# Performance work log

Measured on AMD Instinct MI355X. Metric: run time of the kernel, lower is better.

Reference implementation:

```python
import jax, jax.numpy as jnp
import numpy as np

N_NODES = 100000
N_EDGES = 1600000
NUM_FEATURES = 128


def setup_inputs() -> dict:
    key = jax.random.key(0)
    ks = jax.random.split(key, 10)
    x = jax.random.normal(ks[0], (N_NODES, NUM_FEATURES), dtype=jnp.float32)
    edge_index = jax.random.randint(ks[1], (2, N_EDGES), 0, N_NODES, dtype=jnp.int64)
    # conv1 MLP: Linear(num_features,128) -> ReLU -> Linear(128,128)
    s1 = 1.0 / np.sqrt(NUM_FEATURES)
    W1 = jax.random.uniform(ks[2], (NUM_FEATURES, 128), jnp.float32, -s1, s1)
    b1 = jax.random.uniform(ks[3], (128,), jnp.float32, -s1, s1)
    s2 = 1.0 / np.sqrt(128)
    W2 = jax.random.uniform(ks[4], (128, 128), jnp.float32, -s2, s2)
    b2 = jax.random.uniform(ks[5], (128,), jnp.float32, -s2, s2)
    # conv2 MLP: Linear(128,64) -> ReLU -> Linear(64,64)
    W3 = jax.random.uniform(ks[6], (128, 64), jnp.float32, -s2, s2)
    b3 = jax.random.uniform(ks[7], (64,), jnp.float32, -s2, s2)
    s3 = 1.0 / np.sqrt(64)
    W4 = jax.random.uniform(ks[8], (64, 64), jnp.float32, -s3, s3)
    b4 = jax.random.uniform(ks[9], (64,), jnp.float32, -s3, s3)
    return {"x": x, "edge_index": edge_index, "W1": W1, "b1": b1,
            "W2": W2, "b2": b2, "W3": W3, "b3": b3, "W4": W4, "b4": b4}


def _gin_conv(x, src, dst, Wa, ba, Wb, bb):
    # GINConv with eps=0: out = MLP(x + sum_{j->i} x_j)
    agg = jax.ops.segment_sum(x[src], dst, num_segments=N_NODES)
    h = x + agg
    h = jax.nn.relu(h @ Wa + ba)
    return h @ Wb + bb


def reference(x, edge_index, W1, b1, W2, b2, W3, b3, W4, b4):
    src, dst = edge_index[0], edge_index[1]
    h = jax.nn.relu(_gin_conv(x, src, dst, W1, b1, W2, b2))
    h = jax.nn.relu(_gin_conv(h, src, dst, W3, b3, W4, b4))
    return h
```

## Files before the change

### kernel.cpp

```cpp
#include <hip/hip_runtime.h>
#include <hip/hip_bf16.h>

#define NODES 100000
#define EDGES 1600000
#define NBINS ((NODES + 127) >> 7)
#define BINCAP 4096
#define PB_BLOCKS 256
#define PB_CHUNK ((EDGES + PB_BLOCKS - 1) / PB_BLOCKS)
#define CAST_BLOCKS 12500
#define WPREP_BLOCKS 176

typedef __bf16 bf16x8 __attribute__((ext_vector_type(8)));
typedef float f32x4 __attribute__((ext_vector_type(4)));

__device__ __forceinline__ unsigned short f2b(float f) {
  __hip_bfloat16 h = __float2bfloat16(f);
  return __builtin_bit_cast(unsigned short, h);
}
__device__ __forceinline__ float b_lo(unsigned u) { return __uint_as_float(u << 16); }
__device__ __forceinline__ float b_hi(unsigned u) { return __uint_as_float(u & 0xffff0000u); }

__global__ __launch_bounds__(256) void prep_count(
    const float4* __restrict__ x4, ushort4* __restrict__ xh4,
    const float* __restrict__ W1, const float* __restrict__ W2,
    const float* __restrict__ W3, const float* __restrict__ W4,
    unsigned short* __restrict__ Wt1, unsigned short* __restrict__ Wt2,
    unsigned short* __restrict__ Wt3, unsigned short* __restrict__ Wt4,
    const int* __restrict__ dst, int* __restrict__ partialT) {
  __shared__ int h[NBINS];
  const int b = blockIdx.x;
  if (b < CAST_BLOCKS) {
    int i = b * 256 + threadIdx.x;
    float4 v = x4[i];
    ushort4 o;
    o.x = f2b(v.x); o.y = f2b(v.y); o.z = f2b(v.z); o.w = f2b(v.w);
    xh4[i] = o;
    return;
  }
  if (b < CAST_BLOCKS + WPREP_BLOCKS) {
    int i = (b - CAST_BLOCKS) * 256 + threadIdx.x;
    if (i < 16384) {
      int n = i >> 7, k = i & 127;
      Wt1[i] = f2b(W1[k * 128 + n]);
    } else if (i < 32768) {
      int j = i - 16384; int n = j >> 7, k = j & 127;
      Wt2[j] = f2b(W2[k * 128 + n]);
    } else if (i < 40960) {
      int j = i - 32768; int n = j >> 7, k = j & 127;
      Wt3[j] = f2b(W3[k * 64 + n]);
    } else if (i < 45056) {
      int j = i - 40960; int n = j >> 6, k = j & 63;
      Wt4[j] = f2b(W4[k * 64 + n]);
    }
    return;
  }
  const int cb = b - CAST_BLOCKS - WPREP_BLOCKS;
  for (int i = threadIdx.x; i < NBINS; i += 256) h[i] = 0;
  __syncthreads();
  const int beg = cb * PB_CHUNK;
  const int end = min(beg + PB_CHUNK, EDGES);
  for (int e = beg + threadIdx.x; e < end; e += 256)
    atomicAdd(&h[dst[e] >> 7], 1);
  __syncthreads();
  for (int i = threadIdx.x; i < NBINS; i += 256)
    partialT[i * PB_BLOCKS + cb] = h[i];
}

__global__ __launch_bounds__(256) void scan_blockoff(const int* __restrict__ partialT,
                                                     int* __restrict__ blockoffT,
                                                     int* __restrict__ binTotal) {
  __shared__ int s[256];
  const int bin = blockIdx.x;
  const int t = threadIdx.x;
  int v = partialT[bin * PB_BLOCKS + t];
  s[t] = v;
  __syncthreads();
  for (int off = 1; off < 256; off <<= 1) {
    int u = (t >= off) ? s[t - off] : 0;
    __syncthreads();
    s[t] += u;
    __syncthreads();
  }
  blockoffT[bin * PB_BLOCKS + t] = s[t] - v;
  if (t == 255) binTotal[bin] = s[255];
}

__global__ __launch_bounds__(1024) void scan_totals(const int* __restrict__ binTotal,
                                                    int* __restrict__ binStart,
                                                    int* __restrict__ rowstart) {
  __shared__ int s[1024];
  const int t = threadIdx.x;
  int v = (t < NBINS) ? binTotal[t] : 0;
  s[t] = v;
  __syncthreads();
  for (int off = 1; off < 1024; off <<= 1) {
    int u = (t >= off) ? s[t - off] : 0;
    __syncthreads();
    s[t] += u;
    __syncthreads();
  }
  if (t < NBINS) binStart[t] = s[t] - v;
  if (t == 0) {
    binStart[NBINS] = EDGES;
    rowstart[NODES] = EDGES;
  }
}

__global__ __launch_bounds__(256) void bin_scatter(const int* __restrict__ src,
                                                   const int* __restrict__ dst,
                                                   const int* __restrict__ binStart,
                                                   const int* __restrict__ blockoffT,
                                                   unsigned* __restrict__ coarse) {
  __shared__ int base[NBINS];
  __shared__ int h[NBINS];
  const int beg = blockIdx.x * PB_CHUNK;
  const int end = min(beg + PB_CHUNK, EDGES);
  for (int i = threadIdx.x; i < NBINS; i += 256) {
    base[i] = binStart[i] + blockoffT[i * PB_BLOCKS + blockIdx.x];
    h[i] = 0;
  }
  __syncthreads();
  for (int e = beg + threadIdx.x; e < end; e += 256) {
    int d = dst[e];
    int b = d >> 7;
    int pos = base[b] + atomicAdd(&h[b], 1);
    coarse[pos] = (unsigned)src[e] | ((unsigned)(d & 127) << 17);
  }
}

__global__ __launch_bounds__(256) void bin_fine(const unsigned* __restrict__ coarse,
                                                const int* __restrict__ binStart,
                                                int* __restrict__ rowstart,
                                                int* __restrict__ bucket) {
  __shared__ unsigned ent[BINCAP];
  __shared__ unsigned obuf[BINCAP];
  __shared__ int deg[128];
  __shared__ int pre[128];
  const int b = blockIdx.x;
  const int t = threadIdx.x;
  const int s0 = binStart[b];
  const int nE = binStart[b + 1] - s0;
  const int binBase = b << 7;

  if (t < 128) deg[t] = 0;
  __syncthreads();
  for (int i = t; i < nE; i += 256) {
    unsigned e = coarse[s0 + i];
    ent[i] = e;
    atomicAdd(&deg[e >> 17], 1);
  }
  __syncthreads();
  int v = 0;
  if (t < 128) {
    v = deg[t];
    pre[t] = v;
  }
  __syncthreads();
  for (int off = 1; off < 128; off <<= 1) {
    int u = (t >= off && t < 128) ? pre[t - off] : 0;
    __syncthreads();
    if (t < 128) pre[t] += u;
    __syncthreads();
  }
  if (t < 128) {
    int ex = pre[t] - v;
    if (binBase + t < NODES) rowstart[binBase + t] = s0 + ex;
    deg[t] = ex;
  }
  __syncthreads();
  for (int i = t; i < nE; i += 256) {
    unsigned e = ent[i];
    int pos = atomicAdd(&deg[e >> 17], 1);
    obuf[pos] = e & 0x1FFFFu;
  }
  __syncthreads();
  for (int i = t; i < nE; i += 256) bucket[s0 + i] = (int)obuf[i];
}

__global__ __launch_bounds__(256) void gather_sum_bf16(
    const uint4* __restrict__ xq, const int* __restrict__ rowstart,
    const int* __restrict__ bucket, uint4* __restrict__ outq) {
  const int n = blockIdx.x * 4 + (threadIdx.x >> 6);
  if (n >= NODES) return;
  const int lane = threadIdx.x & 63;
  const int g = lane >> 4;
  const int fl = lane & 15;

  float a[8] = {0.f, 0.f, 0.f, 0.f, 0.f, 0.f, 0.f, 0.f};
  if (g == 0) {
    uint4 v = xq[(size_t)n * 16 + fl];
    a[0] = b_lo(v.x); a[1] = b_hi(v.x);
    a[2] = b_lo(v.y); a[3] = b_hi(v.y);
    a[4] = b_lo(v.z); a[5] = b_hi(v.z);
    a[6] = b_lo(v.w); a[7] = b_hi(v.w);
  }

  const int beg = rowstart[n];
  const int end = rowstart[n + 1];
  for (int j = beg; j < end; j += 16) {
    int e0 = j + g, e1 = j + 4 + g, e2 = j + 8 + g, e3 = j + 12 + g;
    int i0 = (e0 < end) ? e0 : (end - 1);
    int i1 = (e1 < end) ? e1 : (end - 1);
    int i2 = (e2 < end) ? e2 : (end - 1);
    int i3 = (e3 < end) ? e3 : (end - 1);
    int s0 = bucket[i0], s1 = bucket[i1], s2 = bucket[i2], s3 = bucket[i3];
    uint4 v0 = xq[(size_t)s0 * 16 + fl];
    uint4 v1 = xq[(size_t)s1 * 16 + fl];
    uint4 v2 = xq[(size_t)s2 * 16 + fl];
    uint4 v3 = xq[(size_t)s3 * 16 + fl];
    float m0 = (e0 < end) ? 1.f : 0.f;
    float m1 = (e1 < end) ? 1.f : 0.f;
    float m2 = (e2 < end) ? 1.f : 0.f;
    float m3 = (e3 < end) ? 1.f : 0.f;
    a[0] = fmaf(b_lo(v0.x), m0, a[0]); a[1] = fmaf(b_hi(v0.x), m0, a[1]);
    a[2] = fmaf(b_lo(v0.y), m0, a[2]); a[3] = fmaf(b_hi(v0.y), m0, a[3]);
    a[4] = fmaf(b_lo(v0.z), m0, a[4]); a[5] = fmaf(b_hi(v0.z), m0, a[5]);
    a[6] = fmaf(b_lo(v0.w), m0, a[6]); a[7] = fmaf(b_hi(v0.w), m0, a[7]);
    a[0] = fmaf(b_lo(v1.x), m1, a[0]); a[1] = fmaf(b_hi(v1.x), m1, a[1]);
    a[2] = fmaf(b_lo(v1.y), m1, a[2]); a[3] = fmaf(b_hi(v1.y), m1, a[3]);
    a[4] = fmaf(b_lo(v1.z), m1, a[4]); a[5] = fmaf(b_hi(v1.z), m1, a[5]);
    a[6] = fmaf(b_lo(v1.w), m1, a[6]); a[7] = fmaf(b_hi(v1.w), m1, a[7]);
    a[0] = fmaf(b_lo(v2.x), m2, a[0]); a[1] = fmaf(b_hi(v2.x), m2, a[1]);
    a[2] = fmaf(b_lo(v2.y), m2, a[2]); a[3] = fmaf(b_hi(v2.y), m2, a[3]);
    a[4] = fmaf(b_lo(v2.z), m2, a[4]); a[5] = fmaf(b_hi(v2.z), m2, a[5]);
    a[6] = fmaf(b_lo(v2.w), m2, a[6]); a[7] = fmaf(b_hi(v2.w), m2, a[7]);
    a[0] = fmaf(b_lo(v3.x), m3, a[0]); a[1] = fmaf(b_hi(v3.x), m3, a[1]);
    a[2] = fmaf(b_lo(v3.y), m3, a[2]); a[3] = fmaf(b_hi(v3.y), m3, a[3]);
    a[4] = fmaf(b_lo(v3.z), m3, a[4]); a[5] = fmaf(b_hi(v3.z), m3, a[5]);
    a[6] = fmaf(b_lo(v3.w), m3, a[6]); a[7] = fmaf(b_hi(v3.w), m3, a[7]);
  }

#pragma unroll
  for (int k = 0; k < 8; k++) {
    a[k] += __shfl_xor(a[k], 16, 64);
    a[k] += __shfl_xor(a[k], 32, 64);
  }

  if (lane < 16) {
    uint4 o;
    o.x = ((unsigned)f2b(a[1]) << 16) | f2b(a[0]);
    o.y = ((unsigned)f2b(a[3]) << 16) | f2b(a[2]);
    o.z = ((unsigned)f2b(a[5]) << 16) | f2b(a[4]);
    o.w = ((unsigned)f2b(a[7]) << 16) | f2b(a[6]);
    outq[(size_t)n * 16 + fl] = o;
  }
}

template <int K, int N1, int N2, bool OUT_F32>
__global__ __launch_bounds__(256, 3) void mlp_fused(
    const unsigned short* __restrict__ A,
    const unsigned short* __restrict__ Wa, const float* __restrict__ ba,
    const unsigned short* __restrict__ Wb, const float* __restrict__ bb,
    void* __restrict__ Cout, int M) {
  constexpr int LDA = K + 8;
  constexpr int LWA = K + 8;
  constexpr int LWB = N1 + 8;
  constexpr int NT1 = N1 / 16, KB1 = K / 32;
  constexpr int NT2 = N2 / 16, KB2 = N1 / 32;
  constexpr int WSH = (N1 * LWA > N2 * LWB) ? N1 * LWA : N2 * LWB;
  __shared__ unsigned short S[64 * LDA];
  __shared__ unsigned short Wl[WSH];

  const int tid = threadIdx.x;
  const int wave = tid >> 6;
  const int lane = tid & 63;
  const int g = lane >> 4;
  const int fl = lane & 15;
  const int rowBase = blockIdx.x * 64;

  for (int i = tid; i < 64 * (K / 8); i += 256) {
    int r = i / (K / 8), c = i % (K / 8);
    uint4 v = make_uint4(0, 0, 0, 0);
    if (rowBase + r < M)
      v = ((const uint4*)A)[(size_t)(rowBase + r) * (K / 8) + c];
    *(uint4*)&S[r * LDA + c * 8] = v;
  }
  for (int i = tid; i < N1 * (K / 8); i += 256) {
    int n = i / (K / 8), c = i % (K / 8);
    *(uint4*)&Wl[n * LWA + c * 8] = *(const uint4*)&Wa[(size_t)n * K + c * 8];
  }
  __syncthreads();

  const int arow = wave * 16 + fl;

  f32x4 acc[NT1];
#pragma unroll
  for (int c = 0; c < NT1; c++) acc[c] = (f32x4){0.f, 0.f, 0.f, 0.f};
#pragma unroll
  for (int kb = 0; kb < KB1; kb++) {
    bf16x8 av = *(const bf16x8*)&S[arow * LDA + kb * 32 + g * 8];
#pragma unroll
    for (int c = 0; c < NT1; c++) {
      bf16x8 bv = *(const bf16x8*)&Wl[(c * 16 + fl) * LWA + kb * 32 + g * 8];
      acc[c] = __builtin_amdgcn_mfma_f32_16x16x32_bf16(av, bv, acc[c], 0, 0, 0);
    }
  }

#pragma unroll
  for (int c = 0; c < NT1; c++) {
    int col = c * 16 + fl;
    float bv = ba[col];
#pragma unroll
    for (int reg = 0; reg < 4; reg++) {
      int rloc = wave * 16 + g * 4 + reg;
      S[rloc * LDA + col] = f2b(fmaxf(acc[c][reg] + bv, 0.f));
    }
  }
  __syncthreads();

  for (int i = tid; i < N2 * (N1 / 8); i += 256) {
    int n = i / (N1 / 8), c = i % (N1 / 8);
    *(uint4*)&Wl[n * LWB + c * 8] = *(const uint4*)&Wb[(size_t)n * N1 + c * 8];
  }
  __syncthreads();

  f32x4 acc2[NT2];
#pragma unroll
  for (int c = 0; c < NT2; c++) acc2[c] = (f32x4){0.f, 0.f, 0.f, 0.f};
#pragma unroll
  for (int kb = 0; kb < KB2; kb++) {
    bf16x8 av = *(const bf16x8*)&S[arow * LDA + kb * 32 + g * 8];
#pragma unroll
    for (int c = 0; c < NT2; c++) {
      bf16x8 bv = *(const bf16x8*)&Wl[(c * 16 + fl) * LWB + kb * 32 + g * 8];
      acc2[c] = __builtin_amdgcn_mfma_f32_16x16x32_bf16(av, bv, acc2[c], 0, 0, 0);
    }
  }

#pragma unroll
  for (int c = 0; c < NT2; c++) {
    int col = c * 16 + fl;
    float bv = bb[col];
#pragma unroll
    for (int reg = 0; reg < 4; reg++) {
      int row = rowBase + wave * 16 + g * 4 + reg;
      if (row < M) {
        float v = fmaxf(acc2[c][reg] + bv, 0.f);
        if (OUT_F32)
          ((float*)Cout)[(size_t)row * N2 + col] = v;
        else
          ((unsigned short*)Cout)[(size_t)row * N2 + col] = f2b(v);
      }
    }
  }
}

extern "C" void kernel_launch(void* const* d_in, const int* in_sizes, int n_in,
                              void* d_out, int out_size, void* d_ws, size_t ws_size,
                              hipStream_t stream) {
  const float* x = (const float*)d_in[0];
  const int* ei = (const int*)d_in[1];
  const int* src = ei;
  const int* dst = ei + EDGES;
  const float* W1 = (const float*)d_in[2];
  const float* b1 = (const float*)d_in[3];
  const float* W2 = (const float*)d_in[4];
  const float* b2 = (const float*)d_in[5];
  const float* W3 = (const float*)d_in[6];
  const float* b3 = (const float*)d_in[7];
  const float* W4 = (const float*)d_in[8];
  const float* b4 = (const float*)d_in[9];
  float* out = (float*)d_out;

  char* ws = (char*)d_ws;
  unsigned short* xh = (unsigned short*)ws;
  unsigned short* hA = xh + (size_t)NODES * 128;
  unsigned short* hB = hA + (size_t)NODES * 128;
  unsigned short* Wt1 = hB + (size_t)NODES * 128;
  unsigned short* Wt2 = Wt1 + 128 * 128;
  unsigned short* Wt3 = Wt2 + 128 * 128;
  unsigned short* Wt4 = Wt3 + 64 * 128;
  int* rowstart = (int*)(Wt4 + 64 * 64);
  int* binStart = rowstart + NODES + 1;
  int* binTotal = binStart + NBINS + 1;
  int* partialT = binTotal + NBINS;
  int* blockoffT = partialT + NBINS * PB_BLOCKS;
  unsigned* coarse = (unsigned*)(blockoffT + NBINS * PB_BLOCKS);
  int* bucket = (int*)(coarse + EDGES);

  const int nblocks4 = (NODES + 3) / 4;
  const int gblocks = (NODES + 63) / 64;

  prep_count<<<CAST_BLOCKS + WPREP_BLOCKS + PB_BLOCKS, 256, 0, stream>>>(
      (const float4*)x, (ushort4*)xh, W1, W2, W3, W4, Wt1, Wt2, Wt3, Wt4,
      dst, partialT);
  scan_blockoff<<<NBINS, 256, 0, stream>>>(partialT, blockoffT, binTotal);
  scan_totals<<<1, 1024, 0, stream>>>(binTotal, binStart, rowstart);
  bin_scatter<<<PB_BLOCKS, 256, 0, stream>>>(src, dst, binStart, blockoffT, coarse);
  bin_fine<<<NBINS, 256, 0, stream>>>(coarse, binStart, rowstart, bucket);

  gather_sum_bf16<<<nblocks4, 256, 0, stream>>>((const uint4*)xh, rowstart, bucket,
                                                (uint4*)hA);
  mlp_fused<128, 128, 128, false><<<gblocks, 256, 0, stream>>>(
      hA, Wt1, b1, Wt2, b2, hB, NODES);

  gather_sum_bf16<<<nblocks4, 256, 0, stream>>>((const uint4*)hB, rowstart, bucket,
                                                (uint4*)hA);
  mlp_fused<128, 64, 64, true><<<gblocks, 256, 0, stream>>>(
      hA, Wt3, b3, Wt4, b4, out, NODES);
}
```

Baseline: 341.0 us.

## Gather features in column-chunked bf16 layout so each slice fits in cache

Node features are now stored in a chunk-major layout: 8 slices of 16 bf16 columns, each slice 3.2 MB. The gather kernel processes one slice per block group (blockIdx & 7), so the random source-row reads hit a working set small enough for L2/LLC. The cast, the MLP input load and the hidden-layer store are rewritten to use this layout. The cost is re-reading the CSR indices eight times, with more blocks and shorter per-lane 32-byte loads. It also uses nontemporal loads for the index streams.

```diff
diff --git a/kernel.cpp b/kernel.cpp
--- a/kernel.cpp
+++ b/kernel.cpp
@@ -10,8 +10,13 @@
 #define CAST_BLOCKS 12500
 #define WPREP_BLOCKS 176
 
+#define NCHUNK 8
+#define CHUNK_U4 (NODES * 2)
+#define GS_BLOCKS (NCHUNK * (NODES / 16))
+
 typedef __bf16 bf16x8 __attribute__((ext_vector_type(8)));
 typedef float f32x4 __attribute__((ext_vector_type(4)));
+typedef unsigned u32x4 __attribute__((ext_vector_type(4)));
 
 __device__ __forceinline__ unsigned short f2b(float f) {
   __hip_bfloat16 h = __float2bfloat16(f);
@@ -30,11 +35,15 @@
   __shared__ int h[NBINS];
   const int b = blockIdx.x;
   if (b < CAST_BLOCKS) {
-    int i = b * 256 + threadIdx.x;
-    float4 v = x4[i];
-    ushort4 o;
-    o.x = f2b(v.x); o.y = f2b(v.y); o.z = f2b(v.z); o.w = f2b(v.w);
-    xh4[i] = o;
+    int o = b * 256 + threadIdx.x;
+    int c = o / (NODES * 4);
+    int rem = o - c * (NODES * 4);
+    int node = rem >> 2;
+    int q = o & 3;
+    float4 v = x4[node * 32 + c * 4 + q];
+    ushort4 t;
+    t.x = f2b(v.x); t.y = f2b(v.y); t.z = f2b(v.z); t.w = f2b(v.w);
+    xh4[o] = t;
     return;
   }
   if (b < CAST_BLOCKS + WPREP_BLOCKS) {
@@ -177,72 +186,55 @@
   for (int i = t; i < nE; i += 256) bucket[s0 + i] = (int)obuf[i];
 }
 
-__global__ __launch_bounds__(256) void gather_sum_bf16(
-    const uint4* __restrict__ xq, const int* __restrict__ rowstart,
-    const int* __restrict__ bucket, uint4* __restrict__ outq) {
-  const int n = blockIdx.x * 4 + (threadIdx.x >> 6);
-  if (n >= NODES) return;
+__global__ __launch_bounds__(256) void gather_sum_chunk(
+    const unsigned short* __restrict__ xcm, const int* __restrict__ rowstart,
+    const int* __restrict__ bucket, unsigned short* __restrict__ ocm) {
+  const int c = blockIdx.x & 7;
+  const int ngrp = blockIdx.x >> 3;
   const int lane = threadIdx.x & 63;
-  const int g = lane >> 4;
-  const int fl = lane & 15;
+  const int wave = threadIdx.x >> 6;
+  const int n = ngrp * 16 + wave * 4 + (lane >> 4);
+  const int g = (lane >> 1) & 7;
+  const int fl = lane & 1;
+
+  const uint4* slice = (const uint4*)(xcm + (size_t)c * NODES * 16);
+
+  const int beg = __builtin_nontemporal_load(rowstart + n);
+  const int end = __builtin_nontemporal_load(rowstart + n + 1);
 
   float a[8] = {0.f, 0.f, 0.f, 0.f, 0.f, 0.f, 0.f, 0.f};
   if (g == 0) {
-    uint4 v = xq[(size_t)n * 16 + fl];
+    uint4 v = slice[n * 2 + fl];
     a[0] = b_lo(v.x); a[1] = b_hi(v.x);
     a[2] = b_lo(v.y); a[3] = b_hi(v.y);
     a[4] = b_lo(v.z); a[5] = b_hi(v.z);
     a[6] = b_lo(v.w); a[7] = b_hi(v.w);
   }
 
-  const int beg = rowstart[n];
-  const int end = rowstart[n + 1];
-  for (int j = beg; j < end; j += 16) {
-    int e0 = j + g, e1 = j + 4 + g, e2 = j + 8 + g, e3 = j + 12 + g;
-    int i0 = (e0 < end) ? e0 : (end - 1);
-    int i1 = (e1 < end) ? e1 : (end - 1);
-    int i2 = (e2 < end) ? e2 : (end - 1);
-    int i3 = (e3 < end) ? e3 : (end - 1);
-    int s0 = bucket[i0], s1 = bucket[i1], s2 = bucket[i2], s3 = bucket[i3];
-    uint4 v0 = xq[(size_t)s0 * 16 + fl];
-    uint4 v1 = xq[(size_t)s1 * 16 + fl];
-    uint4 v2 = xq[(size_t)s2 * 16 + fl];
-    uint4 v3 = xq[(size_t)s3 * 16 + fl];
-    float m0 = (e0 < end) ? 1.f : 0.f;
-    float m1 = (e1 < end) ? 1.f : 0.f;
-    float m2 = (e2 < end) ? 1.f : 0.f;
-    float m3 = (e3 < end) ? 1.f : 0.f;
-    a[0] = fmaf(b_lo(v0.x), m0, a[0]); a[1] = fmaf(b_hi(v0.x), m0, a[1]);
-    a[2] = fmaf(b_lo(v0.y), m0, a[2]); a[3] = fmaf(b_hi(v0.y), m0, a[3]);
-    a[4] = fmaf(b_lo(v0.z), m0, a[4]); a[5] = fmaf(b_hi(v0.z), m0, a[5]);
-    a[6] = fmaf(b_lo(v0.w), m0, a[6]); a[7] = fmaf(b_hi(v0.w), m0, a[7]);
-    a[0] = fmaf(b_lo(v1.x), m1, a[0]); a[1] = fmaf(b_hi(v1.x), m1, a[1]);
-    a[2] = fmaf(b_lo(v1.y), m1, a[2]); a[3] = fmaf(b_hi(v1.y), m1, a[3]);
-    a[4] = fmaf(b_lo(v1.z), m1, a[4]); a[5] = fmaf(b_hi(v1.z), m1, a[5]);
-    a[6] = fmaf(b_lo(v1.w), m1, a[6]); a[7] = fmaf(b_hi(v1.w), m1, a[7]);
-    a[0] = fmaf(b_lo(v2.x), m2, a[0]); a[1] = fmaf(b_hi(v2.x), m2, a[1]);
-    a[2] = fmaf(b_lo(v2.y), m2, a[2]); a[3] = fmaf(b_hi(v2.y), m2, a[3]);
-    a[4] = fmaf(b_lo(v2.z), m2, a[4]); a[5] = fmaf(b_hi(v2.z), m2, a[5]);
-    a[6] = fmaf(b_lo(v2.w), m2, a[6]); a[7] = fmaf(b_hi(v2.w), m2, a[7]);
-    a[0] = fmaf(b_lo(v3.x), m3, a[0]); a[1] = fmaf(b_hi(v3.x), m3, a[1]);
-    a[2] = fmaf(b_lo(v3.y), m3, a[2]); a[3] = fmaf(b_hi(v3.y), m3, a[3]);
-    a[4] = fmaf(b_lo(v3.z), m3, a[4]); a[5] = fmaf(b_hi(v3.z), m3, a[5]);
-    a[6] = fmaf(b_lo(v3.w), m3, a[6]); a[7] = fmaf(b_hi(v3.w), m3, a[7]);
+  for (int e = beg + g; e < end; e += 8) {
+    int s = __builtin_nontemporal_load(bucket + e);
+    uint4 v = slice[s * 2 + fl];
+    a[0] += b_lo(v.x); a[1] += b_hi(v.x);
+    a[2] += b_lo(v.y); a[3] += b_hi(v.y);
+    a[4] += b_lo(v.z); a[5] += b_hi(v.z);
+    a[6] += b_lo(v.w); a[7] += b_hi(v.w);
   }
 
 #pragma unroll
   for (int k = 0; k < 8; k++) {
-    a[k] += __shfl_xor(a[k], 16, 64);
-    a[k] += __shfl_xor(a[k], 32, 64);
-  }
-
-  if (lane < 16) {
-    uint4 o;
-    o.x = ((unsigned)f2b(a[1]) << 16) | f2b(a[0]);
-    o.y = ((unsigned)f2b(a[3]) << 16) | f2b(a[2]);
-    o.z = ((unsigned)f2b(a[5]) << 16) | f2b(a[4]);
-    o.w = ((unsigned)f2b(a[7]) << 16) | f2b(a[6]);
-    outq[(size_t)n * 16 + fl] = o;
+    a[k] += __shfl_xor(a[k], 2, 64);
+    a[k] += __shfl_xor(a[k], 4, 64);
+    a[k] += __shfl_xor(a[k], 8, 64);
+  }
+
+  if (g == 0) {
+    u32x4 o;
+    o[0] = ((unsigned)f2b(a[1]) << 16) | f2b(a[0]);
+    o[1] = ((unsigned)f2b(a[3]) << 16) | f2b(a[2]);
+    o[2] = ((unsigned)f2b(a[5]) << 16) | f2b(a[4]);
+    o[3] = ((unsigned)f2b(a[7]) << 16) | f2b(a[6]);
+    u32x4* dst4 = (u32x4*)(ocm + (size_t)c * NODES * 16) + (n * 2 + fl);
+    __builtin_nontemporal_store(o, dst4);
   }
 }
 
@@ -269,15 +261,18 @@
   const int rowBase = blockIdx.x * 64;
 
   for (int i = tid; i < 64 * (K / 8); i += 256) {
-    int r = i / (K / 8), c = i % (K / 8);
+    int cch = i >> 7;
+    int r = (i >> 1) & 63;
+    int half = i & 1;
     uint4 v = make_uint4(0, 0, 0, 0);
-    if (rowBase + r < M)
-      v = ((const uint4*)A)[(size_t)(rowBase + r) * (K / 8) + c];
-    *(uint4*)&S[r * LDA + c * 8] = v;
+    int row = rowBase + r;
+    if (row < M)
+      v = ((const uint4*)A)[(size_t)cch * CHUNK_U4 + row * 2 + half];
+    *(uint4*)&S[r * LDA + cch * 16 + half * 8] = v;
   }
   for (int i = tid; i < N1 * (K / 8); i += 256) {
-    int n = i / (K / 8), c = i % (K / 8);
-    *(uint4*)&Wl[n * LWA + c * 8] = *(const uint4*)&Wa[(size_t)n * K + c * 8];
+    int n = i / (K / 8), cc = i % (K / 8);
+    *(uint4*)&Wl[n * LWA + cc * 8] = *(const uint4*)&Wa[(size_t)n * K + cc * 8];
   }
   __syncthreads();
 
@@ -285,61 +280,62 @@
 
   f32x4 acc[NT1];
 #pragma unroll
-  for (int c = 0; c < NT1; c++) acc[c] = (f32x4){0.f, 0.f, 0.f, 0.f};
+  for (int cc = 0; cc < NT1; cc++) acc[cc] = (f32x4){0.f, 0.f, 0.f, 0.f};
 #pragma unroll
   for (int kb = 0; kb < KB1; kb++) {
     bf16x8 av = *(const bf16x8*)&S[arow * LDA + kb * 32 + g * 8];
 #pragma unroll
-    for (int c = 0; c < NT1; c++) {
-      bf16x8 bv = *(const bf16x8*)&Wl[(c * 16 + fl) * LWA + kb * 32 + g * 8];
-      acc[c] = __builtin_amdgcn_mfma_f32_16x16x32_bf16(av, bv, acc[c], 0, 0, 0);
-    }
-  }
-
-#pragma unroll
-  for (int c = 0; c < NT1; c++) {
-    int col = c * 16 + fl;
+    for (int cc = 0; cc < NT1; cc++) {
+      bf16x8 bv = *(const bf16x8*)&Wl[(cc * 16 + fl) * LWA + kb * 32 + g * 8];
+      acc[cc] = __builtin_amdgcn_mfma_f32_16x16x32_bf16(av, bv, acc[cc], 0, 0, 0);
+    }
+  }
+
+#pragma unroll
+  for (int cc = 0; cc < NT1; cc++) {
+    int col = cc * 16 + fl;
     float bv = ba[col];
 #pragma unroll
     for (int reg = 0; reg < 4; reg++) {
       int rloc = wave * 16 + g * 4 + reg;
-      S[rloc * LDA + col] = f2b(fmaxf(acc[c][reg] + bv, 0.f));
+      S[rloc * LDA + col] = f2b(fmaxf(acc[cc][reg] + bv, 0.f));
     }
   }
   __syncthreads();
 
   for (int i = tid; i < N2 * (N1 / 8); i += 256) {
-    int n = i / (N1 / 8), c = i % (N1 / 8);
-    *(uint4*)&Wl[n * LWB + c * 8] = *(const uint4*)&Wb[(size_t)n * N1 + c * 8];
+    int n = i / (N1 / 8), cc = i % (N1 / 8);
+    *(uint4*)&Wl[n * LWB + cc * 8] = *(const uint4*)&Wb[(size_t)n * N1 + cc * 8];
   }
   __syncthreads();
 
   f32x4 acc2[NT2];
 #pragma unroll
-  for (int c = 0; c < NT2; c++) acc2[c] = (f32x4){0.f, 0.f, 0.f, 0.f};
+  for (int cc = 0; cc < NT2; cc++) acc2[cc] = (f32x4){0.f, 0.f, 0.f, 0.f};
 #pragma unroll
   for (int kb = 0; kb < KB2; kb++) {
     bf16x8 av = *(const bf16x8*)&S[arow * LDA + kb * 32 + g * 8];
 #pragma unroll
-    for (int c = 0; c < NT2; c++) {
-      bf16x8 bv = *(const bf16x8*)&Wl[(c * 16 + fl) * LWB + kb * 32 + g * 8];
-      acc2[c] = __builtin_amdgcn_mfma_f32_16x16x32_bf16(av, bv, acc2[c], 0, 0, 0);
-    }
-  }
-
-#pragma unroll
-  for (int c = 0; c < NT2; c++) {
-    int col = c * 16 + fl;
+    for (int cc = 0; cc < NT2; cc++) {
+      bf16x8 bv = *(const bf16x8*)&Wl[(cc * 16 + fl) * LWB + kb * 32 + g * 8];
+      acc2[cc] = __builtin_amdgcn_mfma_f32_16x16x32_bf16(av, bv, acc2[cc], 0, 0, 0);
+    }
+  }
+
+#pragma unroll
+  for (int cc = 0; cc < NT2; cc++) {
+    int col = cc * 16 + fl;
     float bv = bb[col];
 #pragma unroll
     for (int reg = 0; reg < 4; reg++) {
       int row = rowBase + wave * 16 + g * 4 + reg;
       if (row < M) {
-        float v = fmaxf(acc2[c][reg] + bv, 0.f);
+        float v = fmaxf(acc2[cc][reg] + bv, 0.f);
         if (OUT_F32)
           ((float*)Cout)[(size_t)row * N2 + col] = v;
         else
-          ((unsigned short*)Cout)[(size_t)row * N2 + col] = f2b(v);
+          ((unsigned short*)Cout)[(size_t)(col >> 4) * (NODES * 16) +
+                                  (size_t)row * 16 + (col & 15)] = f2b(v);
       }
     }
   }
@@ -378,7 +374,6 @@
   unsigned* coarse = (unsigned*)(blockoffT + NBINS * PB_BLOCKS);
   int* bucket = (int*)(coarse + EDGES);
 
-  const int nblocks4 = (NODES + 3) / 4;
   const int gblocks = (NODES + 63) / 64;
 
   prep_count<<<CAST_BLOCKS + WPREP_BLOCKS + PB_BLOCKS, 256, 0, stream>>>(
@@ -389,13 +384,11 @@
   bin_scatter<<<PB_BLOCKS, 256, 0, stream>>>(src, dst, binStart, blockoffT, coarse);
   bin_fine<<<NBINS, 256, 0, stream>>>(coarse, binStart, rowstart, bucket);
 
-  gather_sum_bf16<<<nblocks4, 256, 0, stream>>>((const uint4*)xh, rowstart, bucket,
-                                                (uint4*)hA);
+  gather_sum_chunk<<<GS_BLOCKS, 256, 0, stream>>>(xh, rowstart, bucket, hA);
   mlp_fused<128, 128, 128, false><<<gblocks, 256, 0, stream>>>(
       hA, Wt1, b1, Wt2, b2, hB, NODES);
 
-  gather_sum_bf16<<<nblocks4, 256, 0, stream>>>((const uint4*)hB, rowstart, bucket,
-                                                (uint4*)hA);
+  gather_sum_chunk<<<GS_BLOCKS, 256, 0, stream>>>(hB, rowstart, bucket, hA);
   mlp_fused<128, 64, 64, true><<<gblocks, 256, 0, stream>>>(
       hA, Wt3, b3, Wt4, b4, out, NODES);
 }
```

Result: slower. 467.2 us (+37.0%).

## Replace two-pass scan CSR build with fixed-capacity bins and global atomic offsets

Applied to the files above, without the earlier changes.

Removes the per-block histogram pass and both prefix-scan kernels. Edges now go into fixed-capacity per-bin slots, with block offsets claimed by global atomics on a per-bin counter. Row ranges are stored as (start, end) pairs so the gather no longer needs a global contiguous prefix. This cuts two kernel launches and a pass over dst, but bin_scatter now reads dst twice. It also relies on no bin exceeding 2560 edges, which holds for uniformly random dst but is not guaranteed in general.

```diff
diff --git a/kernel.cpp b/kernel.cpp
--- a/kernel.cpp
+++ b/kernel.cpp
@@ -4,7 +4,7 @@
 #define NODES 100000
 #define EDGES 1600000
 #define NBINS ((NODES + 127) >> 7)
-#define BINCAP 4096
+#define BINCAP 2560
 #define PB_BLOCKS 256
 #define PB_CHUNK ((EDGES + PB_BLOCKS - 1) / PB_BLOCKS)
 #define CAST_BLOCKS 12500
@@ -26,8 +26,7 @@
     const float* __restrict__ W3, const float* __restrict__ W4,
     unsigned short* __restrict__ Wt1, unsigned short* __restrict__ Wt2,
     unsigned short* __restrict__ Wt3, unsigned short* __restrict__ Wt4,
-    const int* __restrict__ dst, int* __restrict__ partialT) {
-  __shared__ int h[NBINS];
+    int* __restrict__ cnt) {
   const int b = blockIdx.x;
   if (b < CAST_BLOCKS) {
     int i = b * 256 + threadIdx.x;
@@ -54,69 +53,25 @@
     }
     return;
   }
-  const int cb = b - CAST_BLOCKS - WPREP_BLOCKS;
-  for (int i = threadIdx.x; i < NBINS; i += 256) h[i] = 0;
-  __syncthreads();
-  const int beg = cb * PB_CHUNK;
-  const int end = min(beg + PB_CHUNK, EDGES);
-  for (int e = beg + threadIdx.x; e < end; e += 256)
-    atomicAdd(&h[dst[e] >> 7], 1);
-  __syncthreads();
-  for (int i = threadIdx.x; i < NBINS; i += 256)
-    partialT[i * PB_BLOCKS + cb] = h[i];
-}
-
-__global__ __launch_bounds__(256) void scan_blockoff(const int* __restrict__ partialT,
-                                                     int* __restrict__ blockoffT,
-                                                     int* __restrict__ binTotal) {
-  __shared__ int s[256];
-  const int bin = blockIdx.x;
-  const int t = threadIdx.x;
-  int v = partialT[bin * PB_BLOCKS + t];
-  s[t] = v;
-  __syncthreads();
-  for (int off = 1; off < 256; off <<= 1) {
-    int u = (t >= off) ? s[t - off] : 0;
-    __syncthreads();
-    s[t] += u;
-    __syncthreads();
-  }
-  blockoffT[bin * PB_BLOCKS + t] = s[t] - v;
-  if (t == 255) binTotal[bin] = s[255];
-}
-
-__global__ __launch_bounds__(1024) void scan_totals(const int* __restrict__ binTotal,
-                                                    int* __restrict__ binStart,
-                                                    int* __restrict__ rowstart) {
-  __shared__ int s[1024];
-  const int t = threadIdx.x;
-  int v = (t < NBINS) ? binTotal[t] : 0;
-  s[t] = v;
-  __syncthreads();
-  for (int off = 1; off < 1024; off <<= 1) {
-    int u = (t >= off) ? s[t - off] : 0;
-    __syncthreads();
-    s[t] += u;
-    __syncthreads();
-  }
-  if (t < NBINS) binStart[t] = s[t] - v;
-  if (t == 0) {
-    binStart[NBINS] = EDGES;
-    rowstart[NODES] = EDGES;
-  }
+  for (int i = threadIdx.x; i < NBINS; i += 256) cnt[i] = 0;
 }
 
 __global__ __launch_bounds__(256) void bin_scatter(const int* __restrict__ src,
                                                    const int* __restrict__ dst,
-                                                   const int* __restrict__ binStart,
-                                                   const int* __restrict__ blockoffT,
+                                                   int* __restrict__ cnt,
                                                    unsigned* __restrict__ coarse) {
   __shared__ int base[NBINS];
   __shared__ int h[NBINS];
   const int beg = blockIdx.x * PB_CHUNK;
   const int end = min(beg + PB_CHUNK, EDGES);
+  for (int i = threadIdx.x; i < NBINS; i += 256) h[i] = 0;
+  __syncthreads();
+  for (int e = beg + threadIdx.x; e < end; e += 256)
+    atomicAdd(&h[dst[e] >> 7], 1);
+  __syncthreads();
   for (int i = threadIdx.x; i < NBINS; i += 256) {
-    base[i] = binStart[i] + blockoffT[i * PB_BLOCKS + blockIdx.x];
+    int c = h[i];
+    if (c > 0) base[i] = atomicAdd(&cnt[i], c);
     h[i] = 0;
   }
   __syncthreads();
@@ -124,13 +79,13 @@
     int d = dst[e];
     int b = d >> 7;
     int pos = base[b] + atomicAdd(&h[b], 1);
-    coarse[pos] = (unsigned)src[e] | ((unsigned)(d & 127) << 17);
+    coarse[(size_t)b * BINCAP + pos] = (unsigned)src[e] | ((unsigned)(d & 127) << 17);
   }
 }
 
 __global__ __launch_bounds__(256) void bin_fine(const unsigned* __restrict__ coarse,
-                                                const int* __restrict__ binStart,
-                                                int* __restrict__ rowstart,
+                                                const int* __restrict__ cnt,
+                                                int2* __restrict__ rowpairs,
                                                 int* __restrict__ bucket) {
   __shared__ unsigned ent[BINCAP];
   __shared__ unsigned obuf[BINCAP];
@@ -138,8 +93,8 @@
   __shared__ int pre[128];
   const int b = blockIdx.x;
   const int t = threadIdx.x;
-  const int s0 = binStart[b];
-  const int nE = binStart[b + 1] - s0;
+  const int s0 = b * BINCAP;
+  const int nE = cnt[b];
   const int binBase = b << 7;
 
   if (t < 128) deg[t] = 0;
@@ -163,8 +118,9 @@
     __syncthreads();
   }
   if (t < 128) {
-    int ex = pre[t] - v;
-    if (binBase + t < NODES) rowstart[binBase + t] = s0 + ex;
+    int inc = pre[t];
+    int ex = inc - v;
+    if (binBase + t < NODES) rowpairs[binBase + t] = make_int2(s0 + ex, s0 + inc);
     deg[t] = ex;
   }
   __syncthreads();
@@ -178,7 +134,7 @@
 }
 
 __global__ __launch_bounds__(256) void gather_sum_bf16(
-    const uint4* __restrict__ xq, const int* __restrict__ rowstart,
+    const uint4* __restrict__ xq, const int2* __restrict__ rowpairs,
     const int* __restrict__ bucket, uint4* __restrict__ outq) {
   const int n = blockIdx.x * 4 + (threadIdx.x >> 6);
   if (n >= NODES) return;
@@ -195,8 +151,9 @@
     a[6] = b_lo(v.w); a[7] = b_hi(v.w);
   }
 
-  const int beg = rowstart[n];
-  const int end = rowstart[n + 1];
+  const int2 se = rowpairs[n];
+  const int beg = se.x;
+  const int end = se.y;
   for (int j = beg; j < end; j += 16) {
     int e0 = j + g, e1 = j + 4 + g, e2 = j + 8 + g, e3 = j + 12 + g;
     int i0 = (e0 < end) ? e0 : (end - 1);
@@ -370,31 +327,24 @@
   unsigned short* Wt2 = Wt1 + 128 * 128;
   unsigned short* Wt3 = Wt2 + 128 * 128;
   unsigned short* Wt4 = Wt3 + 64 * 128;
-  int* rowstart = (int*)(Wt4 + 64 * 64);
-  int* binStart = rowstart + NODES + 1;
-  int* binTotal = binStart + NBINS + 1;
-  int* partialT = binTotal + NBINS;
-  int* blockoffT = partialT + NBINS * PB_BLOCKS;
-  unsigned* coarse = (unsigned*)(blockoffT + NBINS * PB_BLOCKS);
-  int* bucket = (int*)(coarse + EDGES);
+  int2* rowpairs = (int2*)(Wt4 + 64 * 64);
+  int* cnt = (int*)(rowpairs + NODES);
+  unsigned* coarse = (unsigned*)(cnt + 784);
+  int* bucket = (int*)(coarse + (size_t)NBINS * BINCAP);
 
   const int nblocks4 = (NODES + 3) / 4;
   const int gblocks = (NODES + 63) / 64;
 
-  prep_count<<<CAST_BLOCKS + WPREP_BLOCKS + PB_BLOCKS, 256, 0, stream>>>(
-      (const float4*)x, (ushort4*)xh, W1, W2, W3, W4, Wt1, Wt2, Wt3, Wt4,
-      dst, partialT);
-  scan_blockoff<<<NBINS, 256, 0, stream>>>(partialT, blockoffT, binTotal);
-  scan_totals<<<1, 1024, 0, stream>>>(binTotal, binStart, rowstart);
-  bin_scatter<<<PB_BLOCKS, 256, 0, stream>>>(src, dst, binStart, blockoffT, coarse);
-  bin_fine<<<NBINS, 256, 0, stream>>>(coarse, binStart, rowstart, bucket);
-
-  gather_sum_bf16<<<nblocks4, 256, 0, stream>>>((const uint4*)xh, rowstart, bucket,
+  prep_count<<<CAST_BLOCKS + WPREP_BLOCKS + 1, 256, 0, stream>>>(
+      (const float4*)x, (ushort4*)xh, W1, W2, W3, W4, Wt1, Wt2, Wt3, Wt4, cnt);
+  bin_scatter<<<PB_BLOCKS, 256, 0, stream>>>(src, dst, cnt, coarse);
+  bin_fine<<<NBINS, 256, 0, stream>>>(coarse, cnt, rowpairs, bucket);
+
+  gather_sum_bf16<<<nblocks4, 256, 0, stream>>>((const uint4*)xh, rowpairs, bucket,
                                                 (uint4*)hA);
   mlp_fused<128, 128, 128, false><<<gblocks, 256, 0, stream>>>(
       hA, Wt1, b1, Wt2, b2, hB, NODES);
-
-  gather_sum_bf16<<<nblocks4, 256, 0, stream>>>((const uint4*)hB, rowstart, bucket,
+  gather_sum_bf16<<<nblocks4, 256, 0, stream>>>((const uint4*)hB, rowpairs, bucket,
                                                 (uint4*)hA);
   mlp_fused<128, 64, 64, true><<<gblocks, 256, 0, stream>>>(
       hA, Wt3, b3, Wt4, b4, out, NODES);
```

Result: faster. 328.4 us (-3.7%).
